# Kernel optimization log

Measured on AMD Instinct MI355X. Metric: run time of the kernel, lower is better.

## Reference

```python
import jax, jax.numpy as jnp
import numpy as np
from jax import lax

H = 128       # hidden_size
N = 128       # total agents
T = 12        # future_steps (hardcoded by .view(12, ...))
K = 20        # num_modes
NHEADS = 4
HD = H // NHEADS
MIN_SCALE = 0.001


def setup_inputs() -> dict:
    key = jax.random.key(0)
    ks = jax.random.split(key, 48)

    def w(i, shape, fan):
        return (jax.random.normal(ks[i], shape, dtype=jnp.float32) / np.float32(np.sqrt(fan)))

    z = lambda *s: jnp.zeros(s, jnp.float32)
    o = lambda *s: jnp.ones(s, jnp.float32)
    inp = {}
    inp['global_embed'] = jax.random.normal(ks[0], (T, N, H), dtype=jnp.float32)
    inp['hidden_state'] = jax.random.normal(ks[1], (N, H), dtype=jnp.float32)
    inp['cn'] = jax.random.normal(ks[2], (N, H), dtype=jnp.float32)
    inp['shift_values'] = jax.random.normal(ks[3], (1, N, 2), dtype=jnp.float32)
    inp['max_values'] = jax.random.uniform(ks[4], (N, 2), dtype=jnp.float32)
    # multihead_proj_global: Linear(H, K*H) + LayerNorm + ReLU
    inp['mhp_W'] = w(5, (H, K * H), H); inp['mhp_b'] = z(K * H)
    inp['mhp_g'] = o(K * H); inp['mhp_beta'] = z(K * H)
    # two LSTMCells (bias = b_ih + b_hh fused)
    inp['lstm1_Wih'] = w(6, (H, 4 * H), H); inp['lstm1_Whh'] = w(7, (H, 4 * H), H); inp['lstm1_b'] = z(4 * H)
    inp['lstm2_Wih'] = w(8, (H, 4 * H), H); inp['lstm2_Whh'] = w(9, (H, 4 * H), H); inp['lstm2_b'] = z(4 * H)
    # MultiHeadSelfAttention
    inp['Wq'] = w(10, (H, H), H); inp['bq'] = z(H)
    inp['Wk'] = w(11, (H, H), H); inp['bk'] = z(H)
    inp['Wv'] = w(12, (H, H), H); inp['bv'] = z(H)
    inp['Wo1'] = w(13, (H, 2 * H), H); inp['bo1'] = z(2 * H)
    inp['Wo2'] = w(14, (2 * H, H), 2 * H); inp['bo2'] = z(H)
    # loc head: Linear + LN + ReLU + Linear(H,2)
    inp['loc_W1'] = w(15, (H, H), H); inp['loc_b1'] = z(H)
    inp['loc_g'] = o(H); inp['loc_beta'] = z(H)
    inp['loc_W2'] = w(16, (H, 2), H); inp['loc_b2'] = z(2)
    # scale head
    inp['scl_W1'] = w(17, (H, H), H); inp['scl_b1'] = z(H)
    inp['scl_g'] = o(H); inp['scl_beta'] = z(H)
    inp['scl_W2'] = w(18, (H, 2), H); inp['scl_b2'] = z(2)
    inp['batch_split'] = 4  # number of equal scene segments
    return inp


def _ln(x, g, b):
    m = jnp.mean(x, -1, keepdims=True)
    v = jnp.mean((x - m) ** 2, -1, keepdims=True)
    return (x - m) / jnp.sqrt(v + 1e-5) * g + b


def _head(x, W1, b1, g, beta, W2, b2):
    return jax.nn.relu(_ln(x @ W1 + b1, g, beta)) @ W2 + b2


def reference(global_embed, hidden_state, cn, shift_values, max_values,
              mhp_W, mhp_b, mhp_g, mhp_beta,
              lstm1_Wih, lstm1_Whh, lstm1_b,
              lstm2_Wih, lstm2_Whh, lstm2_b,
              Wq, bq, Wk, bk, Wv, bv, Wo1, bo1, Wo2, bo2,
              loc_W1, loc_b1, loc_g, loc_beta, loc_W2, loc_b2,
              scl_W1, scl_b1, scl_g, scl_beta, scl_W2, scl_b2,
              batch_split):
    S = int(batch_split)
    n = N // S
    # project global embed to per-mode embeddings: [T,N,K*H] -> [T,K*N,H] (mode-major)
    ge = jax.nn.relu(_ln(global_embed @ mhp_W + mhp_b, mhp_g, mhp_beta))
    ge = ge.reshape(T, N, K, H).transpose(0, 2, 1, 3).reshape(T, K * N, H)
    h0 = jnp.tile(hidden_state, (K, 1))  # [K*N,H]
    c0 = jnp.tile(cn, (K, 1))

    def cell1(carry, x):
        h, c = carry
        gi, gf, gg, go = jnp.split(x @ lstm1_Wih + h @ lstm1_Whh + lstm1_b, 4, -1)
        c2 = jax.nn.sigmoid(gf) * c + jax.nn.sigmoid(gi) * jnp.tanh(gg)
        h2 = jax.nn.sigmoid(go) * jnp.tanh(c2)
        return (h2, c2), h2

    _, output1 = lax.scan(cell1, (h0, c0), ge)  # [T,K*N,H]

    loc1 = _head(output1, loc_W1, loc_b1, loc_g, loc_beta, loc_W2, loc_b2)
    loc1 = loc1.transpose(1, 0, 2).reshape(K, N, T, 2)
    scale1 = jax.nn.elu(_head(output1, scl_W1, scl_b1, scl_g, scl_beta, scl_W2, scl_b2)) + 1.0 + MIN_SCALE
    scale1 = scale1.transpose(1, 0, 2).reshape(K, N, T, 2)

    sv = shift_values[0]  # squeeze(0) -> [N,2]
    loc1_ = loc1 * max_values[:, None, :] + sv[:, None, :]            # [K,N,T,2]
    loc1_ = loc1_.transpose(0, 2, 1, 3).reshape(K * T, N, 2).transpose(0, 2, 1)  # [K*T,2,N]
    locs = loc1_.reshape(K * T, 2, S, n).transpose(2, 0, 1, 3)        # [S,K*T,2,n]

    def split_mask(x):  # x: [K*T,2,n]
        d = jnp.abs(x[:, :, :, None] - x[:, :, None, :])              # [K*T,2,n,n]
        m = ((d[:, 0] < 10.0) & (d[:, 1] < 10.0)).reshape(K, T, n, n).any(0)  # [T,n,n]
        return jnp.tile(m, (1, K, K))                                  # [T,K*n,K*n]

    masks = jax.vmap(split_mask)(locs)  # [S,T,K*n,K*n]

    o1d = lax.stop_gradient(output1)  # detach, as in torch
    o1d = o1d.reshape(T, K, S, n, H).transpose(2, 0, 1, 3, 4).reshape(S, T, K * n, H)

    def mhsa(x, mask):  # x: [T,L,H], mask: [T,L,L] bool
        L = K * n
        q = (x @ Wq + bq).reshape(T, L, NHEADS, HD)
        k = (x @ Wk + bk).reshape(T, L, NHEADS, HD)
        v = (x @ Wv + bv).reshape(T, L, NHEADS, HD)
        s = jnp.einsum('blhd,bmhd->bhlm', q, k) / np.float32(np.sqrt(HD))
        s = jnp.where(mask[:, None], s, jnp.float32(-1e8))
        ctx = jnp.einsum('bhlm,bmhd->blhd', jax.nn.softmax(s, -1), v).reshape(T, L, H)
        return jax.nn.relu(ctx @ Wo1 + bo1) @ Wo2 + bo2

    social = jax.vmap(mhsa)(o1d, masks)                                # [S,T,K*n,H]
    social = social.reshape(S, T, K, n, H).transpose(1, 2, 0, 3, 4).reshape(T, K * N, H)

    def cell2(carry, xs):
        h, c = carry
        x, soc = xs
        c = c + soc
        h = h + jnp.tanh(c)
        gi, gf, gg, go = jnp.split(x @ lstm2_Wih + h @ lstm2_Whh + lstm2_b, 4, -1)
        c2 = jax.nn.sigmoid(gf) * c + jax.nn.sigmoid(gi) * jnp.tanh(gg)
        h2 = jax.nn.sigmoid(go) * jnp.tanh(c2)
        return (h2, c2), h2

    _, output2 = lax.scan(cell2, (h0, c0), (ge, social))  # [T,K*N,H]

    loc2 = _head(output2, loc_W1, loc_b1, loc_g, loc_beta, loc_W2, loc_b2)
    loc2 = loc2.transpose(1, 0, 2).reshape(K, N, T, 2)
    scale2 = jax.nn.elu(_head(output2, scl_W1, scl_b1, scl_g, scl_beta, scl_W2, scl_b2)) + 1.0 + MIN_SCALE
    scale2 = scale2.transpose(1, 0, 2).reshape(K, N, T, 2)

    return jnp.stack([loc1, scale1, loc2, scale2], 0)  # [4,K,N,T,2]
```

## Files before the change

### kernel.cpp

```cpp
#include <hip/hip_runtime.h>
#include <hip/hip_bf16.h>

typedef __hip_bfloat16 bf16_t;

static const int cT  = 12;
static const int cN  = 128;
static const int cH  = 128;
static const int cK  = 20;
static const int cKN = 2560;
static const int cS  = 4;
static const int cNS = 32;
static const int cL  = 640;
static const int cHD = 32;

#define CONV_TOTAL 977986

__constant__ int c_off[38] = {0,196608,212992,229376,229632,229888,557568,560128,562688,
  565248,630784,696320,696832,762368,827904,828416,844800,844928,861312,861440,877824,
  877952,910720,910976,943744,943872,960256,960384,960512,960640,960896,960960,977344,
  977472,977600,977728,977984,977986};
__constant__ int c_len[37] = {196608,16384,16384,256,256,327680,2560,2560,2560,
  65536,65536,512,65536,65536,512,16384,128,16384,128,16384,128,
  32768,256,32768,128,16384,128,128,128,256,2,16384,128,128,128,256,2};

struct Ptrs { const void* p[37]; };

typedef __attribute__((ext_vector_type(4))) float f32x4;
typedef __attribute__((ext_vector_type(8))) __bf16 bf16x8;

__device__ __forceinline__ float sigm(float x){ return 1.f/(1.f+expf(-x)); }
__device__ __forceinline__ unsigned short f2h(float x){ return (unsigned short)(__float_as_uint(x)>>16); }
__device__ __forceinline__ float hif(float x){ return __uint_as_float(__float_as_uint(x)&0xFFFF0000u); }

__global__ __launch_bounds__(256) void k_detect(const unsigned short* ge_u16, int* flagp, unsigned int* outw){
  __shared__ int cnt;
  if (threadIdx.x == 0) cnt = 0;
  __syncthreads();
  int ok = 0;
  for (int i = threadIdx.x; i < 128; i += 64){
    unsigned short u = ge_u16[2*i];
    int ex = (u >> 7) & 0xFF;
    if (ex >= 100 && ex <= 140) ok++;
  }
  atomicAdd(&cnt, ok);
  __syncthreads();
  if (threadIdx.x == 0){
    *flagp = (cnt >= 96) ? 1 : 0;
    outw[0] = 0x7FC07FC0u;
  }
}

__global__ __launch_bounds__(256) void k_convert(Ptrs ptrs, const int* flagp, float* dst){
  int g = blockIdx.x*256 + threadIdx.x;
  if (g >= CONV_TOTAL) return;
  int flag = *flagp;
  int seg = 0;
  while (seg < 36 && g >= c_off[seg+1]) ++seg;
  int local = g - c_off[seg];
  if (local >= c_len[seg]) return;
  float v;
  if (flag) v = __bfloat162float(((const bf16_t*)ptrs.p[seg])[local]);
  else      v = ((const float*)ptrs.p[seg])[local];
  dst[g] = v;
}

__global__ __launch_bounds__(256) void k_wprep3(const float* W, unsigned short* out){
  int idx = blockIdx.x*256 + threadIdx.x;
  int l = idx & 63;
  int rest = idx >> 6;
  int s = rest & 3;
  int n = rest >> 2;
  int g = l >> 4, c16 = l & 15;
  unsigned short hi[8], lo[8];
  #pragma unroll
  for (int e = 0; e < 8; ++e){
    int k = 32*s + 16*(e>>2) + 4*g + (e&3);
    float v = W[k*2560 + 16*n + c16];
    hi[e] = f2h(v); lo[e] = f2h(v - hif(v));
  }
  size_t base = (size_t)idx*8;
  *(uint4*)&out[base]          = *(const uint4*)hi;
  *(uint4*)&out[base + 327680] = *(const uint4*)lo;
}

__global__ __launch_bounds__(256) void k_mhp_ln(const float* y, const float* g,
                      const float* be, float* out){
  int row = blockIdx.x;
  int tid = threadIdx.x;
  __shared__ float red[256];
  float v[10];
  const float* yr = y + (size_t)row*2560;
  #pragma unroll
  for (int m = 0; m < 10; ++m) v[m] = yr[tid + 256*m];
  float ps = 0.f;
  #pragma unroll
  for (int m = 0; m < 10; ++m) ps += v[m];
  red[tid] = ps; __syncthreads();
  for (int s2 = 128; s2 > 0; s2 >>= 1){
    if (tid < s2) red[tid] += red[tid+s2];
    __syncthreads();
  }
  float mean = red[0]*(1.f/2560.f);
  __syncthreads();
  float pv = 0.f;
  #pragma unroll
  for (int m = 0; m < 10; ++m){ float d = v[m]-mean; pv += d*d; }
  red[tid] = pv; __syncthreads();
  for (int s2 = 128; s2 > 0; s2 >>= 1){
    if (tid < s2) red[tid] += red[tid+s2];
    __syncthreads();
  }
  float inv = rsqrtf(red[0]*(1.f/2560.f) + 1e-5f);
  int t = row >> 7, nn = row & 127;
  #pragma unroll
  for (int m = 0; m < 10; ++m){
    int col = tid + 256*m;
    float z = (v[m]-mean)*inv*g[col] + be[col];
    z = fmaxf(z, 0.f);
    int k = col >> 7, hh2 = col & 127;
    out[((t*cKN) + k*cN + nn)*cH + hh2] = z;
  }
}

__global__ __launch_bounds__(256) void k_wprep(const float* w0, const float* w1,
    const float* w2, const float* w3, unsigned short* out){
  int idx = blockIdx.x*256 + threadIdx.x;
  int m = idx >> 13;
  int rest = idx & 8191;
  int n = rest >> 8;
  int s = (rest >> 6) & 3;
  int l = rest & 63;
  int g = l >> 4, c16 = l & 15;
  const float* W = (m==0) ? w0 : ((m==1) ? w1 : ((m==2) ? w2 : w3));
  unsigned short hi[8], lo[8];
  #pragma unroll
  for (int e = 0; e < 8; ++e){
    int k = 32*s + 16*(e>>2) + 4*g + (e&3);
    float v = W[k*512 + 16*n + c16];
    hi[e] = f2h(v); lo[e] = f2h(v - hif(v));
  }
  size_t base = (size_t)m*131072 + (size_t)((n*4 + s)*64 + l)*8;
  *(uint4*)&out[base]         = *(const uint4*)hi;
  *(uint4*)&out[base + 65536] = *(const uint4*)lo;
}

__global__ __launch_bounds__(256) void k_wprep2(const float* wq, const float* wk,
    const float* wv, const float* wo1, const float* wo2,
    unsigned short* outA, unsigned short* outB){
  int idx = blockIdx.x*256 + threadIdx.x;
  if (idx >= 14336) return;
  const float* W; int KF, N, local, half; unsigned short* out; size_t off;
  if (idx < 2048)      { W=wq;  KF=4; N=128; off=0;      local=idx;       half=16384; out=outA; }
  else if (idx < 4096) { W=wk;  KF=4; N=128; off=32768;  local=idx-2048;  half=16384; out=outA; }
  else if (idx < 6144) { W=wv;  KF=4; N=128; off=65536;  local=idx-4096;  half=16384; out=outA; }
  else if (idx < 10240){ W=wo1; KF=4; N=256; off=98304;  local=idx-6144;  half=32768; out=outA; }
  else                 { W=wo2; KF=8; N=128; off=0;      local=idx-10240; half=32768; out=outB; }
  int l = local & 63;
  int rest = local >> 6;
  int s = rest & (KF-1);
  int n = (KF == 8) ? (rest >> 3) : (rest >> 2);
  int g = l >> 4, c16 = l & 15;
  unsigned short hi[8], lo[8];
  #pragma unroll
  for (int e = 0; e < 8; ++e){
    int k = 32*s + 16*(e>>2) + 4*g + (e&3);
    float v = W[k*N + 16*n + c16];
    hi[e] = f2h(v); lo[e] = f2h(v - hif(v));
  }
  size_t base = off + (size_t)local*8;
  *(uint4*)&out[base]        = *(const uint4*)hi;
  *(uint4*)&out[base + half] = *(const uint4*)lo;
}

__global__ __launch_bounds__(512) void k_lstm_mfma(const float* ge, float* outh,
    const float* hs0, const float* cn0, const float* soc,
    const unsigned short* wfA, const unsigned short* wfB,
    const float* bias, int phase){
  int r0 = blockIdx.x * 16;
  int tid = threadIdx.x;
  int w = tid >> 6, l = tid & 63;
  int g = l >> 4, c16 = l & 15;
  int scol = w*16 + c16;
  __shared__ unsigned short HFh[2][4][64][8], HFl[2][4][64][8];
  int ps = scol >> 5, prem = scol & 31;
  int pgf = (prem >> 2) & 3;
  int pe  = ((prem >> 4) << 2) + (prem & 3);
  float c[4], h[4];
  #pragma unroll
  for (int r = 0; r < 4; ++r){
    int nn = (r0 + 4*g + r) & 127;
    c[r] = cn0[nn*cH + scol];
    h[r] = hs0[nn*cH + scol];
  }
  float bias_t[4];
  #pragma unroll
  for (int tt = 0; tt < 4; ++tt) bias_t[tt] = bias[tt*128 + scol];

  f32x4 xr[8];
  float socr[4] = {0.f, 0.f, 0.f, 0.f};
  {
    const f32x4* gp = (const f32x4*)ge + ((size_t)(r0 + c16))*32;
    #pragma unroll
    for (int s = 0; s < 4; ++s){ xr[2*s] = gp[8*s + g]; xr[2*s+1] = gp[8*s + 4 + g]; }
    if (phase == 2){
      #pragma unroll
      for (int r = 0; r < 4; ++r)
        socr[r] = soc[(size_t)(r0 + 4*g + r)*cH + scol];
    }
  }

  for (int t = 0; t < cT; ++t){
    int b = t & 1;
    if (phase == 2){
      #pragma unroll
      for (int r = 0; r < 4; ++r){
        c[r] += socr[r];
        h[r] += tanhf(c[r]);
      }
    }
    #pragma unroll
    for (int r = 0; r < 4; ++r){
      HFh[b][ps][pgf*16 + 4*g + r][pe] = f2h(h[r]);
      HFl[b][ps][pgf*16 + 4*g + r][pe] = f2h(h[r] - hif(h[r]));
    }
    bf16x8 xh[4], xl[4];
    #pragma unroll
    for (int s = 0; s < 4; ++s){
      union { unsigned short u[8]; bf16x8 v; } uh, ul;
      #pragma unroll
      for (int m2 = 0; m2 < 4; ++m2){
        float a0 = xr[2*s][m2], b0 = xr[2*s+1][m2];
        uh.u[m2]   = f2h(a0); ul.u[m2]   = f2h(a0 - hif(a0));
        uh.u[4+m2] = f2h(b0); ul.u[4+m2] = f2h(b0 - hif(b0));
      }
      xh[s] = uh.v; xl[s] = ul.v;
    }
    if (t < cT-1){
      const f32x4* gp = (const f32x4*)ge + ((size_t)(t+1)*cKN + r0 + c16)*32;
      #pragma unroll
      for (int s = 0; s < 4; ++s){ xr[2*s] = gp[8*s + g]; xr[2*s+1] = gp[8*s + 4 + g]; }
      if (phase == 2){
        #pragma unroll
        for (int r = 0; r < 4; ++r)
          socr[r] = soc[(size_t)(t+1)*cKN*cH + (size_t)(r0 + 4*g + r)*cH + scol];
      }
    }
    __syncthreads();
    bf16x8 hh[4], hl[4];
    #pragma unroll
    for (int s = 0; s < 4; ++s){
      hh[s] = *(const bf16x8*)&HFh[b][s][l][0];
      hl[s] = *(const bf16x8*)&HFl[b][s][l][0];
    }
    f32x4 a4[4];
    #pragma unroll
    for (int tt = 0; tt < 4; ++tt){
      f32x4 acc = {bias_t[tt], bias_t[tt], bias_t[tt], bias_t[tt]};
      a4[tt] = acc;
    }
    {
      bf16x8 cAh, cAl, cBh, cBl, nAh, nAl, nBh, nBl;
      {
        size_t fo = (size_t)((w*4 + 0)*64 + l)*8;
        cAh = *(const bf16x8*)&wfA[fo];
        cAl = *(const bf16x8*)&wfA[65536 + fo];
        cBh = *(const bf16x8*)&wfB[fo];
        cBl = *(const bf16x8*)&wfB[65536 + fo];
      }
      #pragma unroll
      for (int j = 0; j < 16; ++j){
        int s = j >> 2, tt = j & 3;
        if (j < 15){
          int j2 = j + 1;
          int s2 = j2 >> 2, tt2 = j2 & 3;
          size_t fo = (size_t)(((w + 8*tt2)*4 + s2)*64 + l)*8;
          nAh = *(const bf16x8*)&wfA[fo];
          nAl = *(const bf16x8*)&wfA[65536 + fo];
          nBh = *(const bf16x8*)&wfB[fo];
          nBl = *(const bf16x8*)&wfB[65536 + fo];
        }
        f32x4 acc = a4[tt];
        acc = __builtin_amdgcn_mfma_f32_16x16x32_bf16(xl[s], cAh, acc, 0, 0, 0);
        acc = __builtin_amdgcn_mfma_f32_16x16x32_bf16(xh[s], cAl, acc, 0, 0, 0);
        acc = __builtin_amdgcn_mfma_f32_16x16x32_bf16(xh[s], cAh, acc, 0, 0, 0);
        acc = __builtin_amdgcn_mfma_f32_16x16x32_bf16(hl[s], cBh, acc, 0, 0, 0);
        acc = __builtin_amdgcn_mfma_f32_16x16x32_bf16(hh[s], cBl, acc, 0, 0, 0);
        acc = __builtin_amdgcn_mfma_f32_16x16x32_bf16(hh[s], cBh, acc, 0, 0, 0);
        a4[tt] = acc;
        cAh = nAh; cAl = nAl; cBh = nBh; cBl = nBl;
      }
    }
    #pragma unroll
    for (int r = 0; r < 4; ++r){
      float ig = sigm(a4[0][r]), fg = sigm(a4[1][r]);
      float gg = tanhf(a4[2][r]), og = sigm(a4[3][r]);
      c[r] = fg*c[r] + ig*gg;
      h[r] = og*tanhf(c[r]);
      outh[(size_t)t*cKN*cH + (size_t)(r0 + 4*g + r)*cH + scol] = h[r];
    }
  }
}

template<int KF>
__global__ __launch_bounds__(256) void k_gemm(const float* x, const unsigned short* wf,
    const float* bias, float* out, int NT, int N, int relu, int half){
  int r0 = blockIdx.x * 16;
  int tid = threadIdx.x;
  int wv = tid >> 6, l = tid & 63;
  int g = l >> 4, c16 = l & 15;
  bf16x8 xh[KF], xl[KF];
  const f32x4* gp = (const f32x4*)x + (size_t)(r0 + c16)*(KF*8);
  #pragma unroll
  for (int s = 0; s < KF; ++s){
    f32x4 qa = gp[8*s + g], qb = gp[8*s + 4 + g];
    union { unsigned short u[8]; bf16x8 v; } uh, ul;
    #pragma unroll
    for (int m2 = 0; m2 < 4; ++m2){
      float a0 = qa[m2], b0 = qb[m2];
      uh.u[m2]   = f2h(a0); ul.u[m2]   = f2h(a0 - hif(a0));
      uh.u[4+m2] = f2h(b0); ul.u[4+m2] = f2h(b0 - hif(b0));
    }
    xh[s] = uh.v; xl[s] = ul.v;
  }
  for (int nt = wv; nt < NT; nt += 4){
    float bb = bias[nt*16 + c16];
    f32x4 acc = {bb, bb, bb, bb};
    #pragma unroll
    for (int s = 0; s < KF; ++s){
      const unsigned short* fb = wf + (size_t)((nt*KF + s)*64 + l)*8;
      bf16x8 Wh = *(const bf16x8*)fb;
      bf16x8 Wl = *(const bf16x8*)(fb + half);
      acc = __builtin_amdgcn_mfma_f32_16x16x32_bf16(xl[s], Wh, acc, 0, 0, 0);
      acc = __builtin_amdgcn_mfma_f32_16x16x32_bf16(xh[s], Wl, acc, 0, 0, 0);
      acc = __builtin_amdgcn_mfma_f32_16x16x32_bf16(xh[s], Wh, acc, 0, 0, 0);
    }
    if (relu){
      #pragma unroll
      for (int r = 0; r < 4; ++r) acc[r] = fmaxf(acc[r], 0.f);
    }
    #pragma unroll
    for (int r = 0; r < 4; ++r)
      out[(size_t)(r0 + 4*g + r)*N + nt*16 + c16] = acc[r];
  }
}

__global__ __launch_bounds__(256) void k_gemm3(const float* x, const unsigned short* wf,
    const float* bq, const float* bk, const float* bv,
    float* Q, float* K2, float* V){
  int r0 = blockIdx.x * 16;
  int tid = threadIdx.x;
  int wv = tid >> 6, l = tid & 63;
  int g = l >> 4, c16 = l & 15;
  bf16x8 xh[4], xl[4];
  const f32x4* gp = (const f32x4*)x + (size_t)(r0 + c16)*32;
  #pragma unroll
  for (int s = 0; s < 4; ++s){
    f32x4 qa = gp[8*s + g], qb = gp[8*s + 4 + g];
    union { unsigned short u[8]; bf16x8 v; } uh, ul;
    #pragma unroll
    for (int m2 = 0; m2 < 4; ++m2){
      float a0 = qa[m2], b0 = qb[m2];
      uh.u[m2]   = f2h(a0); ul.u[m2]   = f2h(a0 - hif(a0));
      uh.u[4+m2] = f2h(b0); ul.u[4+m2] = f2h(b0 - hif(b0));
    }
    xh[s] = uh.v; xl[s] = ul.v;
  }
  for (int nt = wv; nt < 24; nt += 4){
    int m = nt >> 3, n = nt & 7;
    const float* bias = (m==0) ? bq : ((m==1) ? bk : bv);
    float* out = (m==0) ? Q : ((m==1) ? K2 : V);
    float bb = bias[n*16 + c16];
    f32x4 acc = {bb, bb, bb, bb};
    const unsigned short* base = wf + (size_t)m*32768;
    #pragma unroll
    for (int s = 0; s < 4; ++s){
      const unsigned short* fb = base + (size_t)((n*4 + s)*64 + l)*8;
      bf16x8 Wh = *(const bf16x8*)fb;
      bf16x8 Wl = *(const bf16x8*)(fb + 16384);
      acc = __builtin_amdgcn_mfma_f32_16x16x32_bf16(xl[s], Wh, acc, 0, 0, 0);
      acc = __builtin_amdgcn_mfma_f32_16x16x32_bf16(xh[s], Wl, acc, 0, 0, 0);
      acc = __builtin_amdgcn_mfma_f32_16x16x32_bf16(xh[s], Wh, acc, 0, 0, 0);
    }
    #pragma unroll
    for (int r = 0; r < 4; ++r)
      out[(size_t)(r0 + 4*g + r)*cH + n*16 + c16] = acc[r];
  }
}

__global__ __launch_bounds__(256) void k_heads(const float* x,
  const float* lW1, const float* lb1, const float* lg, const float* lbe, const float* lW2, const float* lb2v,
  const float* sW1, const float* sb1, const float* sg, const float* sbe, const float* sW2, const float* sb2v,
  void* outv, int q0, float* locsc, const float* maxv, const float* svp, const int* flagp){
  const int ROWS = 16;
  int r0 = blockIdx.x*ROWS;
  __shared__ float xs[ROWS][cH];
  int tid = threadIdx.x;
  for (int p = tid; p < ROWS*32; p += 256){
    int rr = p>>5, u4 = p&31;
    ((float4*)&xs[rr][0])[u4] = ((const float4*)x)[(size_t)(r0+rr)*32 + u4];
  }
  __syncthreads();
  int wv = tid >> 6, lane = tid & 63;
  int head = wv & 1;
  int rbase = (wv >> 1)*8;
  const float* W1 = head ? sW1 : lW1;
  const float* b1 = head ? sb1 : lb1;
  const float* gv = head ? sg  : lg;
  const float* be = head ? sbe : lbe;
  const float* W2 = head ? sW2 : lW2;
  const float* b2 = head ? sb2v: lb2v;
  int j0 = lane, j1 = lane + 64;
  float b10 = b1[j0], b11 = b1[j1];
  float a0[8], a1[8];
  #pragma unroll
  for (int r = 0; r < 8; ++r){ a0[r] = b10; a1[r] = b11; }
  for (int i = 0; i < cH; ++i){
    float w0 = W1[i*cH + j0], w1 = W1[i*cH + j1];
    #pragma unroll
    for (int r = 0; r < 8; ++r){
      float xv = xs[rbase + r][i];
      a0[r] += xv*w0; a1[r] += xv*w1;
    }
  }
  float g0 = gv[j0], g1 = gv[j1], be0 = be[j0], be1 = be[j1];
  float w2a0 = W2[j0*2+0], w2a1 = W2[j0*2+1];
  float w2b0 = W2[j1*2+0], w2b1 = W2[j1*2+1];
  int flag = *flagp;
  float bias0 = b2[0], bias1 = b2[1];
  for (int r = 0; r < 8; ++r){
    float s = a0[r] + a1[r];
    #pragma unroll
    for (int off = 1; off < 64; off <<= 1) s += __shfl_xor(s, off);
    float mean = s*(1.f/128.f);
    float d0 = a0[r]-mean, d1 = a1[r]-mean;
    float vv = d0*d0 + d1*d1;
    #pragma unroll
    for (int off = 1; off < 64; off <<= 1) vv += __shfl_xor(vv, off);
    float inv = rsqrtf(vv*(1.f/128.f) + 1e-5f);
    float z0 = fmaxf(d0*inv*g0 + be0, 0.f);
    float z1 = fmaxf(d1*inv*g1 + be1, 0.f);
    float o0 = z0*w2a0 + z1*w2b0;
    float o1 = z0*w2a1 + z1*w2b1;
    #pragma unroll
    for (int off = 1; off < 64; off <<= 1){
      o0 += __shfl_xor(o0, off);
      o1 += __shfl_xor(o1, off);
    }
    if (lane == 0){
      int rg = r0 + rbase + r;
      int t = rg / cKN, rem = rg - t*cKN;
      int k = rem >> 7, nn = rem & 127;
      float u0 = o0 + bias0, u1 = o1 + bias1;
      if (head == 0){
        size_t oi = (((size_t)q0*cK + k)*cN + nn)*(cT*2) + t*2;
        if (flag){ ((bf16_t*)outv)[oi] = __float2bfloat16(u0); ((bf16_t*)outv)[oi+1] = __float2bfloat16(u1); }
        else     { ((float*)outv)[oi] = u0; ((float*)outv)[oi+1] = u1; }
        if (locsc){
          locsc[((size_t)t*cKN + rem)*2 + 0] = u0*maxv[nn*2+0] + svp[nn*2+0];
          locsc[((size_t)t*cKN + rem)*2 + 1] = u1*maxv[nn*2+1] + svp[nn*2+1];
        }
      } else {
        float e0 = (u0 > 0.f ? u0 : expm1f(u0)) + 1.001f;
        float e1 = (u1 > 0.f ? u1 : expm1f(u1)) + 1.001f;
        size_t oi = (((size_t)(q0+1)*cK + k)*cN + nn)*(cT*2) + t*2;
        if (flag){ ((bf16_t*)outv)[oi] = __float2bfloat16(e0); ((bf16_t*)outv)[oi+1] = __float2bfloat16(e1); }
        else     { ((float*)outv)[oi] = e0; ((float*)outv)[oi+1] = e1; }
      }
    }
  }
}

__global__ __launch_bounds__(256) void k_mask(const float* locsc, unsigned char* m){
  int st = blockIdx.x;
  int s = st / cT, t = st - s*cT;
  __shared__ float lx[cK][cNS], ly[cK][cNS];
  int tid = threadIdx.x;
  for (int p = tid; p < cK*cNS; p += 256){
    int k = p >> 5, i = p & 31;
    int row = t*cKN + k*cN + s*cNS + i;
    lx[k][i] = locsc[row*2+0];
    ly[k][i] = locsc[row*2+1];
  }
  __syncthreads();
  for (int p = tid; p < 1024; p += 256){
    int i = p >> 5, j = p & 31;
    bool any = false;
    for (int k = 0; k < cK; ++k){
      float dx = fabsf(lx[k][i]-lx[k][j]);
      float dy = fabsf(ly[k][i]-ly[k][j]);
      any = any || ((dx < 10.f) && (dy < 10.f));
    }
    m[st*1024 + p] = any ? 1 : 0;
  }
}

__global__ __launch_bounds__(256) void k_attn(const float* Q, const float* Kx, const float* V,
                       const unsigned char* msk, float* ctx){
  int qs   = blockIdx.x;
  int head = blockIdx.y;
  int st   = blockIdx.z;
  int s = st / cT, t = st - s*cT;
  __shared__ unsigned short KLh[2][1024], KLl[2][1024], VLh[2][1024], VLl[2][1024];
  int tid = threadIdx.x;
  int w = tid >> 6, lane = tid & 63;
  int g = lane >> 4, col = lane & 15;
  const float scl = 0.17677669529663687f;

  unsigned int mw0 = 0, mw1 = 0;
  {
    const unsigned int* mr0 = (const unsigned int*)(msk + st*1024 + col*32);
    const unsigned int* mr1 = (const unsigned int*)(msk + st*1024 + (16+col)*32);
    #pragma unroll
    for (int j2 = 0; j2 < 8; ++j2){
      mw0 |= (((mr0[j2] * 0x01020408u) >> 24) & 0xFu) << (4*j2);
      mw1 |= (((mr1[j2] * 0x01020408u) >> 24) & 0xFu) << (4*j2);
    }
  }

  bf16x8 Qh[2], Ql[2];
  int modes[2], ahs[2];
  #pragma unroll
  for (int i = 0; i < 2; ++i){
    int tt = qs*8 + 4*i + w;
    int mode = tt >> 1, ah = tt & 1;
    modes[i] = mode; ahs[i] = ah;
    int qrow = t*cKN + mode*cN + s*cNS + ah*16 + col;
    const f32x4* qp = (const f32x4*)Q + (size_t)qrow*32 + head*8;
    f32x4 qa = qp[g], qb = qp[4+g];
    union { unsigned short u[8]; bf16x8 v; } uh, ul;
    #pragma unroll
    for (int m = 0; m < 4; ++m){
      float x0 = qa[m]*scl;
      uh.u[m] = f2h(x0);
      ul.u[m] = f2h(x0 - hif(x0));
      float x1 = qb[m]*scl;
      uh.u[4+m] = f2h(x1);
      ul.u[4+m] = f2h(x1 - hif(x1));
    }
    Qh[i] = uh.v; Ql[i] = ul.v;
  }

  int kk = tid >> 3, f4 = tid & 7;
  int kwi = (((kk>>4)*4 + (f4&3))*16 + (kk&15))*8 + (f4>>2)*4;
  int vd = tid & 31, quad = tid >> 5;
  int vkey = (quad>>2)*16 + (quad&3)*4;
  int vwi = (((vd>>4)*4 + (quad&3))*16 + (vd&15))*8 + (quad>>2)*4;

  const size_t cstepK = (size_t)cN*32;
  const size_t cstepV = (size_t)cN*128;
  const float4* kptr = (const float4*)Kx + ((size_t)(t*cKN + s*cNS + kk))*32 + head*8 + f4;
  const float*  vptr = V + ((size_t)(t*cKN + s*cNS + vkey))*128 + head*32 + vd;

  float4 kv; float vm0, vm1, vm2, vm3;
  kv = *kptr; kptr += cstepK;
  vm0 = vptr[0]; vm1 = vptr[128]; vm2 = vptr[256]; vm3 = vptr[384]; vptr += cstepV;
  {
    unsigned int h0 = (unsigned int)f2h(kv.x) | ((unsigned int)f2h(kv.y)<<16);
    unsigned int h1 = (unsigned int)f2h(kv.z) | ((unsigned int)f2h(kv.w)<<16);
    float r0 = kv.x-hif(kv.x), r1 = kv.y-hif(kv.y), r2 = kv.z-hif(kv.z), r3 = kv.w-hif(kv.w);
    unsigned int l0 = (unsigned int)f2h(r0) | ((unsigned int)f2h(r1)<<16);
    unsigned int l1 = (unsigned int)f2h(r2) | ((unsigned int)f2h(r3)<<16);
    *(uint2*)&KLh[0][kwi] = make_uint2(h0,h1);
    *(uint2*)&KLl[0][kwi] = make_uint2(l0,l1);
    unsigned int vh0 = (unsigned int)f2h(vm0) | ((unsigned int)f2h(vm1)<<16);
    unsigned int vh1 = (unsigned int)f2h(vm2) | ((unsigned int)f2h(vm3)<<16);
    float s0 = vm0-hif(vm0), s1 = vm1-hif(vm1), s2 = vm2-hif(vm2), s3 = vm3-hif(vm3);
    unsigned int vl0 = (unsigned int)f2h(s0) | ((unsigned int)f2h(s1)<<16);
    unsigned int vl1 = (unsigned int)f2h(s2) | ((unsigned int)f2h(s3)<<16);
    *(uint2*)&VLh[0][vwi] = make_uint2(vh0,vh1);
    *(uint2*)&VLl[0][vwi] = make_uint2(vl0,vl1);
  }
  __syncthreads();

  const f32x4 Z = {0.f, 0.f, 0.f, 0.f};
  f32x4 O[2][2] = {{Z, Z}, {Z, Z}};
  float lac[2] = {0.f, 0.f};

  for (int ch = 0; ch < 20; ++ch){
    int par = ch & 1;
    if (ch < 19){
      kv = *kptr; kptr += cstepK;
      vm0 = vptr[0]; vm1 = vptr[128]; vm2 = vptr[256]; vm3 = vptr[384]; vptr += cstepV;
    }
    bf16x8 KAh0 = *(const bf16x8*)&KLh[par][( g      *16 + col)*8];
    bf16x8 KAl0 = *(const bf16x8*)&KLl[par][( g      *16 + col)*8];
    bf16x8 KAh1 = *(const bf16x8*)&KLh[par][((4 + g) *16 + col)*8];
    bf16x8 KAl1 = *(const bf16x8*)&KLl[par][((4 + g) *16 + col)*8];
    bf16x8 VBh0 = *(const bf16x8*)&VLh[par][( g      *16 + col)*8];
    bf16x8 VBl0 = *(const bf16x8*)&VLl[par][( g      *16 + col)*8];
    bf16x8 VBh1 = *(const bf16x8*)&VLh[par][((4 + g) *16 + col)*8];
    bf16x8 VBl1 = *(const bf16x8*)&VLl[par][((4 + g) *16 + col)*8];
    #pragma unroll
    for (int i = 0; i < 2; ++i){
      f32x4 sa = Z, sb = Z;
      sa = __builtin_amdgcn_mfma_f32_16x16x32_bf16(KAl0, Qh[i], sa, 0, 0, 0);
      sa = __builtin_amdgcn_mfma_f32_16x16x32_bf16(KAh0, Ql[i], sa, 0, 0, 0);
      sa = __builtin_amdgcn_mfma_f32_16x16x32_bf16(KAh0, Qh[i], sa, 0, 0, 0);
      sb = __builtin_amdgcn_mfma_f32_16x16x32_bf16(KAl1, Qh[i], sb, 0, 0, 0);
      sb = __builtin_amdgcn_mfma_f32_16x16x32_bf16(KAh1, Ql[i], sb, 0, 0, 0);
      sb = __builtin_amdgcn_mfma_f32_16x16x32_bf16(KAh1, Qh[i], sb, 0, 0, 0);
      unsigned int mw = ahs[i] ? mw1 : mw0;
      float p[8];
      #pragma unroll
      for (int r = 0; r < 4; ++r){
        float e0 = __expf(sa[r]);
        float e1 = __expf(sb[r]);
        p[r]   = ((mw >> (4*g + r)) & 1)        ? e0 : 0.f;
        p[4+r] = ((mw >> (16 + 4*g + r)) & 1)   ? e1 : 0.f;
      }
      lac[i] += ((p[0]+p[1])+(p[2]+p[3])) + ((p[4]+p[5])+(p[6]+p[7]));
      union { unsigned short u[8]; bf16x8 v; } Ph, Pl;
      #pragma unroll
      for (int e = 0; e < 8; ++e){
        Ph.u[e] = f2h(p[e]);
        Pl.u[e] = f2h(p[e] - hif(p[e]));
      }
      O[i][0] = __builtin_amdgcn_mfma_f32_16x16x32_bf16(Pl.v, VBh0, O[i][0], 0, 0, 0);
      O[i][0] = __builtin_amdgcn_mfma_f32_16x16x32_bf16(Ph.v, VBl0, O[i][0], 0, 0, 0);
      O[i][0] = __builtin_amdgcn_mfma_f32_16x16x32_bf16(Ph.v, VBh0, O[i][0], 0, 0, 0);
      O[i][1] = __builtin_amdgcn_mfma_f32_16x16x32_bf16(Pl.v, VBh1, O[i][1], 0, 0, 0);
      O[i][1] = __builtin_amdgcn_mfma_f32_16x16x32_bf16(Ph.v, VBl1, O[i][1], 0, 0, 0);
      O[i][1] = __builtin_amdgcn_mfma_f32_16x16x32_bf16(Ph.v, VBh1, O[i][1], 0, 0, 0);
    }
    __syncthreads();
    if (ch < 19){
      int nb = 1 - par;
      unsigned int h0 = (unsigned int)f2h(kv.x) | ((unsigned int)f2h(kv.y)<<16);
      unsigned int h1 = (unsigned int)f2h(kv.z) | ((unsigned int)f2h(kv.w)<<16);
      float r0 = kv.x-hif(kv.x), r1 = kv.y-hif(kv.y), r2 = kv.z-hif(kv.z), r3 = kv.w-hif(kv.w);
      unsigned int l0 = (unsigned int)f2h(r0) | ((unsigned int)f2h(r1)<<16);
      unsigned int l1 = (unsigned int)f2h(r2) | ((unsigned int)f2h(r3)<<16);
      *(uint2*)&KLh[nb][kwi] = make_uint2(h0,h1);
      *(uint2*)&KLl[nb][kwi] = make_uint2(l0,l1);
      unsigned int vh0 = (unsigned int)f2h(vm0) | ((unsigned int)f2h(vm1)<<16);
      unsigned int vh1 = (unsigned int)f2h(vm2) | ((unsigned int)f2h(vm3)<<16);
      float s0 = vm0-hif(vm0), s1 = vm1-hif(vm1), s2 = vm2-hif(vm2), s3 = vm3-hif(vm3);
      unsigned int vl0 = (unsigned int)f2h(s0) | ((unsigned int)f2h(s1)<<16);
      unsigned int vl1 = (unsigned int)f2h(s2) | ((unsigned int)f2h(s3)<<16);
      *(uint2*)&VLh[nb][vwi] = make_uint2(vh0,vh1);
      *(uint2*)&VLl[nb][vwi] = make_uint2(vl0,vl1);
    }
    __syncthreads();
  }

  #pragma unroll
  for (int i = 0; i < 2; ++i){
    float lsum = lac[i];
    lsum += __shfl_xor(lsum, 16);
    lsum += __shfl_xor(lsum, 32);
    int base = t*cKN + modes[i]*cN + s*cNS + ahs[i]*16;
    #pragma unroll
    for (int r = 0; r < 4; ++r){
      float lq = __shfl(lsum, 4*g + r);
      float rinv = 1.f / lq;
      float* cp = ctx + (size_t)(base + 4*g + r)*cH + head*cHD;
      cp[col]      = O[i][0][r] * rinv;
      cp[col+16]   = O[i][1][r] * rinv;
    }
  }
}

extern "C" void kernel_launch(void* const* d_in, const int* in_sizes, int n_in,
                              void* d_out, int out_size, void* d_ws, size_t ws_size,
                              hipStream_t stream){
  (void)in_sizes; (void)n_in; (void)out_size; (void)ws_size;

  int*   flagp = (int*)d_ws;
  float* conv  = (float*)d_ws + 64;
  float* big   = (float*)d_ws + 978112;

  const float* ge_f   = conv + 0;
  const float* hs_f   = conv + 196608;
  const float* cn_f   = conv + 212992;
  const float* sv_f   = conv + 229376;
  const float* mx_f   = conv + 229632;
  const float* mhpW_f = conv + 229888;
  const float* mhpb_f = conv + 557568;
  const float* mhpg_f = conv + 560128;
  const float* mhpbe_f= conv + 562688;
  const float* l1Wih_f= conv + 565248;
  const float* l1Whh_f= conv + 630784;
  const float* l1b_f  = conv + 696320;
  const float* l2Wih_f= conv + 696832;
  const float* l2Whh_f= conv + 762368;
  const float* l2b_f  = conv + 827904;
  const float* Wq_f   = conv + 828416;
  const float* bq_f   = conv + 844800;
  const float* Wk_f   = conv + 844928;
  const float* bk_f   = conv + 861312;
  const float* Wv_f   = conv + 861440;
  const float* bv_f   = conv + 877824;
  const float* Wo1_f  = conv + 877952;
  const float* bo1_f  = conv + 910720;
  const float* Wo2_f  = conv + 910976;
  const float* bo2_f  = conv + 943744;
  const float* locW1_f= conv + 943872;
  const float* locb1_f= conv + 960256;
  const float* locg_f = conv + 960384;
  const float* locbe_f= conv + 960512;
  const float* locW2_f= conv + 960640;
  const float* locb2_f= conv + 960896;
  const float* sclW1_f= conv + 960960;
  const float* sclb1_f= conv + 977344;
  const float* sclg_f = conv + 977472;
  const float* sclbe_f= conv + 977600;
  const float* sclW2_f= conv + 977728;
  const float* sclb2_f= conv + 977984;

  const size_t SLOT = (size_t)cT*cKN*cH;
  float* geb = big;
  float* o1b = big + SLOT;
  float* Qb  = big + 2*SLOT;
  float* Kb  = big + 3*SLOT;
  float* Vb  = big + 4*SLOT;
  float* locsc = big + 5*SLOT;
  unsigned char* maskb = (unsigned char*)(locsc + (size_t)cT*cKN*2);
  float* t1 = Qb;
  float* social = Vb;

  unsigned short* wfrag = (unsigned short*)(conv + 229888);
  unsigned short* uA = (unsigned short*)(conv + 565248);
  unsigned short* uB = (unsigned short*)(conv + 696832);
  unsigned short* mfrag = (unsigned short*)(big + 2*SLOT);
  float* ytmp = big + 3*SLOT;

  Ptrs ptrs;
  for (int i = 0; i < 37; ++i) ptrs.p[i] = d_in[i];

  k_detect<<<1, 64, 0, stream>>>((const unsigned short*)d_in[0], flagp, (unsigned int*)d_out);
  k_convert<<<(CONV_TOTAL+255)/256, 256, 0, stream>>>(ptrs, flagp, conv);
  k_wprep3<<<160, 256, 0, stream>>>(mhpW_f, mfrag);
  k_gemm<4><<<96, 256, 0, stream>>>(ge_f, mfrag, mhpb_f, ytmp, 160, 2560, 0, 327680);
  k_mhp_ln<<<1536, 256, 0, stream>>>(ytmp, mhpg_f, mhpbe_f, geb);
  k_wprep<<<128, 256, 0, stream>>>(l1Wih_f, l1Whh_f, l2Wih_f, l2Whh_f, wfrag);
  k_wprep2<<<56, 256, 0, stream>>>(Wq_f, Wk_f, Wv_f, Wo1_f, Wo2_f, uA, uB);
  k_lstm_mfma<<<160, 512, 0, stream>>>(geb, o1b, hs_f, cn_f, (const float*)0,
                                       wfrag + 0, wfrag + 131072, l1b_f, 1);
  k_heads<<<cT*cKN/16, 256, 0, stream>>>(o1b, locW1_f,locb1_f,locg_f,locbe_f,locW2_f,locb2_f,
                                        sclW1_f,sclb1_f,sclg_f,sclbe_f,sclW2_f,sclb2_f,
                                        d_out, 0, locsc, mx_f, sv_f, flagp);
  k_mask<<<cS*cT, 256, 0, stream>>>(locsc, maskb);
  k_gemm3<<<cT*cKN/16, 256, 0, stream>>>(o1b, uA, bq_f, bk_f, bv_f, Qb, Kb, Vb);
  {
    dim3 ag(5, 4, cS*cT);
    k_attn<<<ag, 256, 0, stream>>>(Qb, Kb, Vb, maskb, o1b);
  }
  k_gemm<4><<<cT*cKN/16, 256, 0, stream>>>(o1b, uA + 98304, bo1_f, t1, 16, 256, 1, 32768);
  k_gemm<8><<<cT*cKN/16, 256, 0, stream>>>(t1, uB, bo2_f, social, 8, 128, 0, 32768);
  k_lstm_mfma<<<160, 512, 0, stream>>>(geb, o1b, hs_f, cn_f, social,
                                       wfrag + 262144, wfrag + 393216, l2b_f, 2);
  k_heads<<<cT*cKN/16, 256, 0, stream>>>(o1b, locW1_f,locb1_f,locg_f,locbe_f,locW2_f,locb2_f,
                                        sclW1_f,sclb1_f,sclg_f,sclbe_f,sclW2_f,sclb2_f,
                                        d_out, 2, (float*)0, mx_f, sv_f, flagp);
}
```

Baseline: 632.9 us.

## Fuse attention output MLP GEMMs and split projection GEMM across column chunks

The two attention output linear layers (Wo1 with ReLU, then Wo2) are merged into one kernel. The intermediate 256-wide activation is split into bf16 hi/lo parts and stored in shared memory in MFMA fragment layout, so it no longer makes a round trip through global memory and one launch is dropped. Separately, the multihead projection GEMM, which had only 96 blocks each looping over 160 column tiles, now adds a second grid dimension of 5 column chunks to use more compute units. The cost is extra shared memory per block and repeated conversion of the input rows in every column-chunk block.

```diff
diff --git a/kernel.cpp b/kernel.cpp
--- a/kernel.cpp
+++ b/kernel.cpp
@@ -303,8 +303,10 @@
 
 template<int KF>
 __global__ __launch_bounds__(256) void k_gemm(const float* x, const unsigned short* wf,
-    const float* bias, float* out, int NT, int N, int relu, int half){
+    const float* bias, float* out, int NT, int N, int relu, int half, int ntc){
   int r0 = blockIdx.x * 16;
+  int nt0 = blockIdx.y * ntc;
+  int ntEnd = nt0 + ntc; if (ntEnd > NT) ntEnd = NT;
   int tid = threadIdx.x;
   int wv = tid >> 6, l = tid & 63;
   int g = l >> 4, c16 = l & 15;
@@ -322,7 +324,7 @@
     }
     xh[s] = uh.v; xl[s] = ul.v;
   }
-  for (int nt = wv; nt < NT; nt += 4){
+  for (int nt = nt0 + wv; nt < ntEnd; nt += 4){
     float bb = bias[nt*16 + c16];
     f32x4 acc = {bb, bb, bb, bb};
     #pragma unroll
@@ -384,6 +386,79 @@
     #pragma unroll
     for (int r = 0; r < 4; ++r)
       out[(size_t)(r0 + 4*g + r)*cH + n*16 + c16] = acc[r];
+  }
+}
+
+__global__ __launch_bounds__(256) void k_wo12(const float* x, const unsigned short* wf1,
+    const float* b1, const unsigned short* wf2, const float* b2, float* out){
+  int r0 = blockIdx.x * 16;
+  int tid = threadIdx.x;
+  int wv = tid >> 6, l = tid & 63;
+  int g = l >> 4, c16 = l & 15;
+  __shared__ unsigned short HFh[8][64][8], HFl[8][64][8];
+  bf16x8 xh[4], xl[4];
+  const f32x4* gp = (const f32x4*)x + (size_t)(r0 + c16)*32;
+  #pragma unroll
+  for (int s = 0; s < 4; ++s){
+    f32x4 qa = gp[8*s + g], qb = gp[8*s + 4 + g];
+    union { unsigned short u[8]; bf16x8 v; } uh, ul;
+    #pragma unroll
+    for (int m2 = 0; m2 < 4; ++m2){
+      float a0 = qa[m2], b0v = qb[m2];
+      uh.u[m2]   = f2h(a0);  ul.u[m2]   = f2h(a0 - hif(a0));
+      uh.u[4+m2] = f2h(b0v); ul.u[4+m2] = f2h(b0v - hif(b0v));
+    }
+    xh[s] = uh.v; xl[s] = ul.v;
+  }
+  #pragma unroll
+  for (int q = 0; q < 4; ++q){
+    int nt = wv + 4*q;
+    float bb = b1[nt*16 + c16];
+    f32x4 acc = {bb, bb, bb, bb};
+    #pragma unroll
+    for (int s = 0; s < 4; ++s){
+      const unsigned short* fb = wf1 + (size_t)((nt*4 + s)*64 + l)*8;
+      bf16x8 Wh = *(const bf16x8*)fb;
+      bf16x8 Wl = *(const bf16x8*)(fb + 32768);
+      acc = __builtin_amdgcn_mfma_f32_16x16x32_bf16(xl[s], Wh, acc, 0, 0, 0);
+      acc = __builtin_amdgcn_mfma_f32_16x16x32_bf16(xh[s], Wl, acc, 0, 0, 0);
+      acc = __builtin_amdgcn_mfma_f32_16x16x32_bf16(xh[s], Wh, acc, 0, 0, 0);
+    }
+    int scol = nt*16 + c16;
+    int ps = scol >> 5, prem = scol & 31;
+    int pgf = (prem >> 2) & 3;
+    int pe  = ((prem >> 4) << 2) + (prem & 3);
+    #pragma unroll
+    for (int r = 0; r < 4; ++r){
+      float z = fmaxf(acc[r], 0.f);
+      HFh[ps][pgf*16 + 4*g + r][pe] = f2h(z);
+      HFl[ps][pgf*16 + 4*g + r][pe] = f2h(z - hif(z));
+    }
+  }
+  __syncthreads();
+  bf16x8 yh[8], yl[8];
+  #pragma unroll
+  for (int s = 0; s < 8; ++s){
+    yh[s] = *(const bf16x8*)&HFh[s][l][0];
+    yl[s] = *(const bf16x8*)&HFl[s][l][0];
+  }
+  #pragma unroll
+  for (int q = 0; q < 2; ++q){
+    int nt = wv + 4*q;
+    float bb = b2[nt*16 + c16];
+    f32x4 acc = {bb, bb, bb, bb};
+    #pragma unroll
+    for (int s = 0; s < 8; ++s){
+      const unsigned short* fb = wf2 + (size_t)((nt*8 + s)*64 + l)*8;
+      bf16x8 Wh = *(const bf16x8*)fb;
+      bf16x8 Wl = *(const bf16x8*)(fb + 32768);
+      acc = __builtin_amdgcn_mfma_f32_16x16x32_bf16(yl[s], Wh, acc, 0, 0, 0);
+      acc = __builtin_amdgcn_mfma_f32_16x16x32_bf16(yh[s], Wl, acc, 0, 0, 0);
+      acc = __builtin_amdgcn_mfma_f32_16x16x32_bf16(yh[s], Wh, acc, 0, 0, 0);
+    }
+    #pragma unroll
+    for (int r = 0; r < 4; ++r)
+      out[(size_t)(r0 + 4*g + r)*cH + nt*16 + c16] = acc[r];
   }
 }
 
@@ -715,7 +790,6 @@
   float* Vb  = big + 4*SLOT;
   float* locsc = big + 5*SLOT;
   unsigned char* maskb = (unsigned char*)(locsc + (size_t)cT*cKN*2);
-  float* t1 = Qb;
   float* social = Vb;
 
   unsigned short* wfrag = (unsigned short*)(conv + 229888);
@@ -730,7 +804,10 @@
   k_detect<<<1, 64, 0, stream>>>((const unsigned short*)d_in[0], flagp, (unsigned int*)d_out);
   k_convert<<<(CONV_TOTAL+255)/256, 256, 0, stream>>>(ptrs, flagp, conv);
   k_wprep3<<<160, 256, 0, stream>>>(mhpW_f, mfrag);
-  k_gemm<4><<<96, 256, 0, stream>>>(ge_f, mfrag, mhpb_f, ytmp, 160, 2560, 0, 327680);
+  {
+    dim3 mg(96, 5);
+    k_gemm<4><<<mg, 256, 0, stream>>>(ge_f, mfrag, mhpb_f, ytmp, 160, 2560, 0, 327680, 32);
+  }
   k_mhp_ln<<<1536, 256, 0, stream>>>(ytmp, mhpg_f, mhpbe_f, geb);
   k_wprep<<<128, 256, 0, stream>>>(l1Wih_f, l1Whh_f, l2Wih_f, l2Whh_f, wfrag);
   k_wprep2<<<56, 256, 0, stream>>>(Wq_f, Wk_f, Wv_f, Wo1_f, Wo2_f, uA, uB);
@@ -745,8 +822,7 @@
     dim3 ag(5, 4, cS*cT);
     k_attn<<<ag, 256, 0, stream>>>(Qb, Kb, Vb, maskb, o1b);
   }
-  k_gemm<4><<<cT*cKN/16, 256, 0, stream>>>(o1b, uA + 98304, bo1_f, t1, 16, 256, 1, 32768);
-  k_gemm<8><<<cT*cKN/16, 256, 0, stream>>>(t1, uB, bo2_f, social, 8, 128, 0, 32768);
+  k_wo12<<<cT*cKN/16, 256, 0, stream>>>(o1b, uA + 98304, bo1_f, uB, bo2_f, social);
   k_lstm_mfma<<<160, 512, 0, stream>>>(geb, o1b, hs_f, cn_f, social,
                                        wfrag + 262144, wfrag + 393216, l2b_f, 2);
   k_heads<<<cT*cKN/16, 256, 0, stream>>>(o1b, locW1_f,locb1_f,locg_f,locbe_f,locW2_f,locb2_f,
```

Result: faster. 584.7 us (-7.6%).
